# Performance work log

Measured on AMD Instinct MI355X. Metric: run time of the kernel, lower is better.

## Reference

```python
import jax, jax.numpy as jnp
import numpy as np

NUM_HEADS = 16
DIM_HEAD = 64
MAX_LEN = 512


def setup_inputs() -> dict:
    key = jax.random.key(0)
    ks = jax.random.split(key, 6)
    B, N, D = 16, 512, 1024
    inner = NUM_HEADS * DIM_HEAD  # 1024
    x = jax.random.normal(ks[0], (B, N, D), dtype=jnp.float32)
    w_qkv = jax.random.normal(ks[1], (D, 3 * inner), dtype=jnp.float32) * (D ** -0.5)
    b_qkv = jnp.zeros((3 * inner,), dtype=jnp.float32)
    rel_emb = jax.random.normal(ks[2], (2 * MAX_LEN - 1, NUM_HEADS), dtype=jnp.float32) * 0.02
    w_out = jax.random.normal(ks[3], (inner, D), dtype=jnp.float32) * (inner ** -0.5)
    b_out = jnp.zeros((D,), dtype=jnp.float32)
    return {"x": x, "w_qkv": w_qkv, "b_qkv": b_qkv, "rel_emb": rel_emb,
            "w_out": w_out, "b_out": b_out}


def reference(x, w_qkv, b_qkv, rel_emb, w_out, b_out):
    B, N, D = x.shape
    h, dh = NUM_HEADS, DIM_HEAD
    scale = dh ** -0.5
    qkv = x @ w_qkv + b_qkv  # (B, N, 3*h*dh)
    q, k, v = jnp.split(qkv, 3, axis=-1)
    def to_heads(t):
        return t.reshape(B, N, h, dh).transpose(0, 2, 1, 3)  # (B, h, N, dh)
    q, k, v = to_heads(q), to_heads(k), to_heads(v)
    dots = jnp.einsum('bhid,bhjd->bhij', q, k) * scale  # (B, h, N, N)
    # relative position bias: emb[(i - j) + max_len - 1] -> (N, N, h) -> (1, h, N, N)
    idx = jnp.arange(N)[:, None] - jnp.arange(N)[None, :] + (MAX_LEN - 1)
    bias = rel_emb[idx].transpose(2, 0, 1)[None]  # (1, h, N, N)
    attn = jax.nn.softmax(dots + bias, axis=-1)
    out = jnp.einsum('bhij,bhjd->bhid', attn, v)  # (B, h, N, dh)
    out = out.transpose(0, 2, 1, 3).reshape(B, N, h * dh)
    return out @ w_out + b_out
```

## Files before the change

kernel.cpp:

```cpp
#include <hip/hip_runtime.h>

#define SEQ    512
#define NH     16
#define DH     64
#define DMODEL 1024
#define NB     16
#define MROWS  (NB*SEQ)
#define MAXL   512

typedef _Float16 f16;
typedef f16  f16x8 __attribute__((ext_vector_type(8)));
typedef f16  f16x4 __attribute__((ext_vector_type(4)));
typedef float f32x4 __attribute__((ext_vector_type(4)));

__device__ static inline void gll16(const f16* g, f16* l) {
    __builtin_amdgcn_global_load_lds(
        (const __attribute__((address_space(1))) void*)(g),
        (__attribute__((address_space(3))) void*)(l), 16, 0, 0);
}

__global__ __launch_bounds__(256)
void prep(const float* __restrict__ x, f16* __restrict__ xh,
          const float* __restrict__ wqkv, f16* __restrict__ wqkvT,
          const float* __restrict__ wout, f16* __restrict__ woutT)
{
    const int bid = blockIdx.x, t = threadIdx.x;
    if (bid < 8192) {
        int i = (bid * 256 + t) * 4;
        float4 v = *(const float4*)(x + i);
        f16x4 h = { (f16)v.x, (f16)v.y, (f16)v.z, (f16)v.w };
        *(f16x4*)(xh + i) = h;
        return;
    }
    __shared__ float tile[32][33];
    const float* in; f16* out; int C, gx, gy;
    if (bid < 8192 + 3072) {
        int b2 = bid - 8192; in = wqkv; out = wqkvT; C = 3072;
        gx = b2 % 96; gy = b2 / 96;
    } else {
        int b2 = bid - 11264; in = wout; out = woutT; C = 1024;
        gx = b2 & 31; gy = b2 >> 5;
    }
    const int R = 1024;
    int tx = t & 31, ty = t >> 5;
    int c0 = gx * 32, r0 = gy * 32;
    #pragma unroll
    for (int i = 0; i < 4; ++i)
        tile[ty + i * 8][tx] = in[(size_t)(r0 + ty + i * 8) * C + c0 + tx];
    __syncthreads();
    #pragma unroll
    for (int i = 0; i < 4; ++i)
        out[(size_t)(c0 + ty + i * 8) * R + r0 + tx] = (f16)tile[tx][ty + i * 8];
}

template<int MODE>
__global__ __launch_bounds__(256)
void gemm_mfma(const f16* __restrict__ A, const f16* __restrict__ Bt,
               const float* __restrict__ bias, int N, int K,
               float* __restrict__ Cout,
               f16* __restrict__ qb, f16* __restrict__ kb, f16* __restrict__ vb)
{
    __shared__ f16 As[128 * 64];
    __shared__ f16 Bs[128 * 64];
    const int t = threadIdx.x;
    const int lane = t & 63, w = t >> 6;
    const int quad = lane >> 4, l16 = lane & 15;
    const int xr = l16 & 7;
    const int m0 = blockIdx.y * 128, n0 = blockIdx.x * 128;
    const int wm = (w & 1) * 64, wn = (w >> 1) * 64;

    f32x4 acc[4][4];
    #pragma unroll
    for (int i = 0; i < 4; ++i)
        #pragma unroll
        for (int j = 0; j < 4; ++j)
            acc[i][j] = f32x4{0.f, 0.f, 0.f, 0.f};

    const int sr8 = lane >> 3;
    const int sc8 = (lane & 7) ^ sr8;
    const f16* agp = A  + (size_t)(m0 + w * 32 + sr8) * K + sc8 * 8;
    const f16* bgp = Bt + (size_t)(n0 + w * 32 + sr8) * K + sc8 * 8;
    f16* asl = As + w * 2048;
    f16* bsl = Bs + w * 2048;

    for (int k0 = 0; k0 < K; k0 += 64) {
        __syncthreads();
        #pragma unroll
        for (int c = 0; c < 4; ++c) {
            gll16(agp + k0 + c * 8 * K, asl + c * 512);
            gll16(bgp + k0 + c * 8 * K, bsl + c * 512);
        }
        __syncthreads();
        #pragma unroll
        for (int ks = 0; ks < 2; ++ks) {
            f16x8 af[4], bf[4];
            #pragma unroll
            for (int ms = 0; ms < 4; ++ms)
                af[ms] = *(const f16x8*)&As[(wm + ms * 16 + l16) * 64
                                            + (((ks * 4 + quad) ^ xr) * 8)];
            #pragma unroll
            for (int ns = 0; ns < 4; ++ns)
                bf[ns] = *(const f16x8*)&Bs[(wn + ns * 16 + l16) * 64
                                            + (((ks * 4 + quad) ^ xr) * 8)];
            #pragma unroll
            for (int ms = 0; ms < 4; ++ms)
                #pragma unroll
                for (int ns = 0; ns < 4; ++ns)
                    acc[ms][ns] = __builtin_amdgcn_mfma_f32_16x16x32_f16(
                        af[ms], bf[ns], acc[ms][ns], 0, 0, 0);
        }
    }

    if (MODE == 0) {
        #pragma unroll
        for (int ns = 0; ns < 4; ++ns) {
            int col = n0 + wn + ns * 16 + l16;
            float bv = bias[col];
            int which = col >> 10;
            int hh = (col & 1023) >> 6, d = col & 63;
            #pragma unroll
            for (int ms = 0; ms < 4; ++ms) {
                int rowb = m0 + wm + ms * 16 + quad * 4;
                int bb_ = rowb >> 9, n_ = rowb & 511;
                if (which == 0) {
                    #pragma unroll
                    for (int reg = 0; reg < 4; ++reg)
                        qb[((size_t)(bb_ * NH + hh) * SEQ + n_ + reg) * DH + d] =
                            (f16)(acc[ms][ns][reg] + bv);
                } else if (which == 2) {
                    f16x4 pk;
                    #pragma unroll
                    for (int reg = 0; reg < 4; ++reg)
                        pk[reg] = (f16)(acc[ms][ns][reg] + bv);
                    int c8s = ((n_ >> 3) & 7) ^ (d & 7);
                    *(f16x4*)(vb + ((size_t)(bb_ * NH + hh) * DH + d) * SEQ
                                 + (n_ & ~63) + c8s * 8 + (n_ & 7)) = pk;
                } else {
                    #pragma unroll
                    for (int reg = 0; reg < 4; ++reg) {
                        int n = n_ + reg;
                        int dd = (((d >> 3) ^ (n & 7)) * 8) + (d & 7);
                        kb[((size_t)(bb_ * NH + hh) * SEQ + n) * DH + dd] =
                            (f16)(acc[ms][ns][reg] + bv);
                    }
                }
            }
        }
    } else {
        #pragma unroll
        for (int ns = 0; ns < 4; ++ns) {
            int col = n0 + wn + ns * 16 + l16;
            float bv = bias[col];
            #pragma unroll
            for (int ms = 0; ms < 4; ++ms) {
                int rowb = m0 + wm + ms * 16 + quad * 4;
                #pragma unroll
                for (int reg = 0; reg < 4; ++reg)
                    Cout[(size_t)(rowb + reg) * N + col] = acc[ms][ns][reg] + bv;
            }
        }
    }
}

__global__ __launch_bounds__(512)
void attn_mfma(const f16* __restrict__ qb, const f16* __restrict__ kb,
               const f16* __restrict__ vb, const float* __restrict__ rel,
               f16* __restrict__ ob)
{
    __shared__ f16 Ks[128 * 64];
    __shared__ f16 Vt[64 * 128];
    __shared__ f16 Pw[8][16 * 64];
    __shared__ float relh[1024];

    const int t = threadIdx.x;
    const int lane = t & 63, w = t >> 6;
    const int quad = lane >> 4, l16 = lane & 15;
    const int xr = l16 & 7;
    const int bh = blockIdx.x;
    const int h = bh & 15, b = bh >> 4;

    for (int i = t; i < 2 * MAXL - 1; i += 512)
        relh[i] = rel[i * NH + h] * 1.44269504f;

    f16x8 qf[4][2];
    #pragma unroll
    for (int c = 0; c < 4; ++c) {
        const f16* qrow = qb + ((size_t)bh * SEQ + w * 64 + c * 16 + l16) * DH + quad * 8;
        qf[c][0] = *(const f16x8*)(qrow);
        qf[c][1] = *(const f16x8*)(qrow + 32);
    }

    f32x4 o[4][4];
    float lsum[4];
    #pragma unroll
    for (int c = 0; c < 4; ++c) {
        lsum[c] = 0.f;
        #pragma unroll
        for (int dt = 0; dt < 4; ++dt) o[c][dt] = f32x4{0.f, 0.f, 0.f, 0.f};
    }

    const f16* kbase = kb + (size_t)bh * SEQ * DH;
    const f16* vbase = vb + (size_t)bh * DH * SEQ;
    f16* pw = &Pw[w][0];

    for (int kt = 0; kt < 4; ++kt) {
        __syncthreads();
        #pragma unroll
        for (int r = 0; r < 2; ++r) {
            const f16* src = kbase + (size_t)(kt * 128 + r * 64 + w * 8 + (lane >> 3)) * DH
                           + (lane & 7) * 8;
            gll16(src, Ks + r * 4096 + w * 512);
        }
        #pragma unroll
        for (int r = 0; r < 2; ++r) {
            const f16* src = vbase + (size_t)(r * 32 + w * 4 + (lane >> 4)) * SEQ
                           + kt * 128 + ((lane & 15) >> 3) * 64 + (lane & 7) * 8;
            gll16(src, Vt + r * 4096 + w * 512);
        }
        __syncthreads();

        #pragma unroll
        for (int c = 0; c < 4; ++c) {
            f32x4 sT[8];
            #pragma unroll
            for (int mt = 0; mt < 8; ++mt) {
                const f16* kr = &Ks[(mt * 16 + l16) * 64];
                f16x8 a0 = *(const f16x8*)(kr + ((quad ^ xr) * 8));
                f16x8 a1 = *(const f16x8*)(kr + (((4 + quad) ^ xr) * 8));
                f32x4 s = f32x4{0.f, 0.f, 0.f, 0.f};
                s = __builtin_amdgcn_mfma_f32_16x16x32_f16(a0, qf[c][0], s, 0, 0, 0);
                s = __builtin_amdgcn_mfma_f32_16x16x32_f16(a1, qf[c][1], s, 0, 0, 0);
                sT[mt] = s;
            }

            const int cb0 = w * 64 + c * 16 + l16 + (MAXL - 1) - kt * 128 - quad * 4;
            #pragma unroll
            for (int g = 0; g < 2; ++g) {
                #pragma unroll
                for (int m4 = 0; m4 < 4; ++m4) {
                    int mt = g * 4 + m4;
                    f16x4 pk;
                    #pragma unroll
                    for (int reg = 0; reg < 4; ++reg) {
                        float e = exp2f(fmaf(sT[mt][reg], 0.180336878f,
                                             relh[cb0 - mt * 16 - reg]));
                        lsum[c] += e;
                        pk[reg] = (f16)e;
                    }
                    int c8 = (m4 * 2 + (quad >> 1)) ^ xr;
                    *(f16x4*)&pw[l16 * 64 + c8 * 8 + (quad & 1) * 4] = pk;
                }
                __builtin_amdgcn_s_waitcnt(0xC07F);

                #pragma unroll
                for (int s2 = 0; s2 < 2; ++s2) {
                    f16x8 pa = *(const f16x8*)&pw[l16 * 64 + (((s2 * 4 + quad) ^ xr) * 8)];
                    #pragma unroll
                    for (int dt = 0; dt < 4; ++dt) {
                        const f16* vr = &Vt[(dt * 16 + l16) * 128 + g * 64];
                        f16x8 vb8 = *(const f16x8*)(vr + (((s2 * 4 + quad) ^ xr) * 8));
                        o[c][dt] = __builtin_amdgcn_mfma_f32_16x16x32_f16(
                            pa, vb8, o[c][dt], 0, 0, 0);
                    }
                }
            }
        }
    }

    #pragma unroll
    for (int c = 0; c < 4; ++c) {
        float ls = lsum[c];
        ls += __shfl_xor(ls, 16, 64);
        ls += __shfl_xor(ls, 32, 64);
        #pragma unroll
        for (int reg = 0; reg < 4; ++reg) {
            float inv = 1.0f / __shfl(ls, quad * 4 + reg, 64);
            size_t rbase = ((size_t)b * SEQ + w * 64 + c * 16 + quad * 4 + reg) * DMODEL
                         + h * DH;
            #pragma unroll
            for (int dt = 0; dt < 4; ++dt)
                ob[rbase + dt * 16 + l16] = (f16)(o[c][dt][reg] * inv);
        }
    }
}

extern "C" void kernel_launch(void* const* d_in, const int* in_sizes, int n_in,
                              void* d_out, int out_size, void* d_ws, size_t ws_size,
                              hipStream_t stream)
{
    const float* x    = (const float*)d_in[0];
    const float* wqkv = (const float*)d_in[1];
    const float* bqkv = (const float*)d_in[2];
    const float* rel  = (const float*)d_in[3];
    const float* wout = (const float*)d_in[4];
    const float* bout = (const float*)d_in[5];
    float* out = (float*)d_out;
    char* ws = (char*)d_ws;

    const size_t XH = (size_t)MROWS * DMODEL;
    f16* xh    = (f16*)(ws);
    f16* wqkvT = (f16*)(ws + 2 * XH);
    f16* woutT = wqkvT + (size_t)3 * DMODEL * DMODEL;
    f16* qbuf  = woutT + (size_t)DMODEL * DMODEL;
    f16* kbuf  = qbuf + XH;
    f16* vbuf  = kbuf + XH;
    f16* abuf  = vbuf + XH;

    prep<<<12288, 256, 0, stream>>>(x, xh, wqkv, wqkvT, wout, woutT);

    gemm_mfma<0><<<dim3(3 * DMODEL / 128, MROWS / 128), 256, 0, stream>>>(
        xh, wqkvT, bqkv, 3 * DMODEL, DMODEL, nullptr, qbuf, kbuf, vbuf);

    attn_mfma<<<NB * NH, 512, 0, stream>>>(qbuf, kbuf, vbuf, rel, abuf);

    gemm_mfma<1><<<dim3(DMODEL / 128, MROWS / 128), 256, 0, stream>>>(
        abuf, woutT, bout, DMODEL, DMODEL, out, nullptr, nullptr, nullptr);
}
```

Before: 230.1 us.

## Fuse x fp16 conversion into QKV GEMM, use 32x32 MFMA, double-buffer attention K/V

```diff
diff --git a/kernel.cpp b/kernel.cpp
--- a/kernel.cpp
+++ b/kernel.cpp
@@ -11,7 +11,8 @@
 typedef _Float16 f16;
 typedef f16  f16x8 __attribute__((ext_vector_type(8)));
 typedef f16  f16x4 __attribute__((ext_vector_type(4)));
-typedef float f32x4 __attribute__((ext_vector_type(4)));
+typedef float f32x4  __attribute__((ext_vector_type(4)));
+typedef float f32x16 __attribute__((ext_vector_type(16)));
 
 __device__ static inline void gll16(const f16* g, f16* l) {
     __builtin_amdgcn_global_load_lds(
@@ -20,25 +21,17 @@
 }
 
 __global__ __launch_bounds__(256)
-void prep(const float* __restrict__ x, f16* __restrict__ xh,
-          const float* __restrict__ wqkv, f16* __restrict__ wqkvT,
+void prep(const float* __restrict__ wqkv, f16* __restrict__ wqkvT,
           const float* __restrict__ wout, f16* __restrict__ woutT)
 {
     const int bid = blockIdx.x, t = threadIdx.x;
-    if (bid < 8192) {
-        int i = (bid * 256 + t) * 4;
-        float4 v = *(const float4*)(x + i);
-        f16x4 h = { (f16)v.x, (f16)v.y, (f16)v.z, (f16)v.w };
-        *(f16x4*)(xh + i) = h;
-        return;
-    }
     __shared__ float tile[32][33];
     const float* in; f16* out; int C, gx, gy;
-    if (bid < 8192 + 3072) {
-        int b2 = bid - 8192; in = wqkv; out = wqkvT; C = 3072;
-        gx = b2 % 96; gy = b2 / 96;
+    if (bid < 3072) {
+        in = wqkv; out = wqkvT; C = 3072;
+        gx = bid % 96; gy = bid / 96;
     } else {
-        int b2 = bid - 11264; in = wout; out = woutT; C = 1024;
+        int b2 = bid - 3072; in = wout; out = woutT; C = 1024;
         gx = b2 & 31; gy = b2 >> 5;
     }
     const int R = 1024;
@@ -53,9 +46,10 @@
         out[(size_t)(c0 + ty + i * 8) * R + r0 + tx] = (f16)tile[tx][ty + i * 8];
 }
 
-template<int MODE>
+template<int MODE, int CVTA>
 __global__ __launch_bounds__(256)
-void gemm_mfma(const f16* __restrict__ A, const f16* __restrict__ Bt,
+void gemm_mfma(const float* __restrict__ A32, const f16* __restrict__ A16,
+               const f16* __restrict__ Bt,
                const float* __restrict__ bias, int N, int K,
                float* __restrict__ Cout,
                f16* __restrict__ qb, f16* __restrict__ kb, f16* __restrict__ vb)
@@ -64,99 +58,125 @@
     __shared__ f16 Bs[128 * 64];
     const int t = threadIdx.x;
     const int lane = t & 63, w = t >> 6;
-    const int quad = lane >> 4, l16 = lane & 15;
-    const int xr = l16 & 7;
+    const int l32 = lane & 31, half = lane >> 5;
     const int m0 = blockIdx.y * 128, n0 = blockIdx.x * 128;
     const int wm = (w & 1) * 64, wn = (w >> 1) * 64;
 
-    f32x4 acc[4][4];
-    #pragma unroll
-    for (int i = 0; i < 4; ++i)
-        #pragma unroll
-        for (int j = 0; j < 4; ++j)
-            acc[i][j] = f32x4{0.f, 0.f, 0.f, 0.f};
+    f32x16 acc[2][2];
+    #pragma unroll
+    for (int i = 0; i < 2; ++i)
+        #pragma unroll
+        for (int j = 0; j < 2; ++j)
+            acc[i][j] = (f32x16)(0.f);
 
     const int sr8 = lane >> 3;
     const int sc8 = (lane & 7) ^ sr8;
-    const f16* agp = A  + (size_t)(m0 + w * 32 + sr8) * K + sc8 * 8;
     const f16* bgp = Bt + (size_t)(n0 + w * 32 + sr8) * K + sc8 * 8;
+    f16* bsl = Bs + w * 2048;
+    const f16* agp = CVTA ? nullptr
+                          : A16 + (size_t)(m0 + w * 32 + sr8) * K + sc8 * 8;
     f16* asl = As + w * 2048;
-    f16* bsl = Bs + w * 2048;
+
+    const int crow = t >> 1, chalf = t & 1;
+    const float* agp32 = CVTA ? A32 + (size_t)(m0 + crow) * K + chalf * 32 : nullptr;
+    const int cr8 = crow & 7;
 
     for (int k0 = 0; k0 < K; k0 += 64) {
         __syncthreads();
         #pragma unroll
-        for (int c = 0; c < 4; ++c) {
-            gll16(agp + k0 + c * 8 * K, asl + c * 512);
+        for (int c = 0; c < 4; ++c)
             gll16(bgp + k0 + c * 8 * K, bsl + c * 512);
+        if (CVTA) {
+            float4 v[8];
+            #pragma unroll
+            for (int i = 0; i < 8; ++i)
+                v[i] = *(const float4*)(agp32 + k0 + i * 4);
+            #pragma unroll
+            for (int c = 0; c < 4; ++c) {
+                f16x8 hh = { (f16)v[2*c].x, (f16)v[2*c].y, (f16)v[2*c].z, (f16)v[2*c].w,
+                             (f16)v[2*c+1].x, (f16)v[2*c+1].y, (f16)v[2*c+1].z, (f16)v[2*c+1].w };
+                int c8 = (chalf * 4 + c) ^ cr8;
+                *(f16x8*)&As[crow * 64 + c8 * 8] = hh;
+            }
+        } else {
+            #pragma unroll
+            for (int c = 0; c < 4; ++c)
+                gll16(agp + k0 + c * 8 * K, asl + c * 512);
         }
         __syncthreads();
-        #pragma unroll
-        for (int ks = 0; ks < 2; ++ks) {
-            f16x8 af[4], bf[4];
-            #pragma unroll
-            for (int ms = 0; ms < 4; ++ms)
-                af[ms] = *(const f16x8*)&As[(wm + ms * 16 + l16) * 64
-                                            + (((ks * 4 + quad) ^ xr) * 8)];
-            #pragma unroll
-            for (int ns = 0; ns < 4; ++ns)
-                bf[ns] = *(const f16x8*)&Bs[(wn + ns * 16 + l16) * 64
-                                            + (((ks * 4 + quad) ^ xr) * 8)];
-            #pragma unroll
-            for (int ms = 0; ms < 4; ++ms)
-                #pragma unroll
-                for (int ns = 0; ns < 4; ++ns)
-                    acc[ms][ns] = __builtin_amdgcn_mfma_f32_16x16x32_f16(
+
+        #pragma unroll
+        for (int ks = 0; ks < 4; ++ks) {
+            f16x8 af[2], bf[2];
+            #pragma unroll
+            for (int ms = 0; ms < 2; ++ms) {
+                int row = wm + ms * 32 + l32;
+                int c8 = (ks * 2 + half) ^ (row & 7);
+                af[ms] = *(const f16x8*)&As[row * 64 + c8 * 8];
+            }
+            #pragma unroll
+            for (int ns = 0; ns < 2; ++ns) {
+                int row = wn + ns * 32 + l32;
+                int c8 = (ks * 2 + half) ^ (row & 7);
+                bf[ns] = *(const f16x8*)&Bs[row * 64 + c8 * 8];
+            }
+            #pragma unroll
+            for (int ms = 0; ms < 2; ++ms)
+                #pragma unroll
+                for (int ns = 0; ns < 2; ++ns)
+                    acc[ms][ns] = __builtin_amdgcn_mfma_f32_32x32x16_f16(
                         af[ms], bf[ns], acc[ms][ns], 0, 0, 0);
         }
     }
 
-    if (MODE == 0) {
-        #pragma unroll
-        for (int ns = 0; ns < 4; ++ns) {
-            int col = n0 + wn + ns * 16 + l16;
-            float bv = bias[col];
+    const int bb_ = m0 >> 9;
+    #pragma unroll
+    for (int ns = 0; ns < 2; ++ns) {
+        int col = n0 + wn + ns * 32 + l32;
+        float bv = bias[col];
+        if (MODE == 0) {
             int which = col >> 10;
             int hh = (col & 1023) >> 6, d = col & 63;
             #pragma unroll
-            for (int ms = 0; ms < 4; ++ms) {
-                int rowb = m0 + wm + ms * 16 + quad * 4;
-                int bb_ = rowb >> 9, n_ = rowb & 511;
-                if (which == 0) {
-                    #pragma unroll
-                    for (int reg = 0; reg < 4; ++reg)
-                        qb[((size_t)(bb_ * NH + hh) * SEQ + n_ + reg) * DH + d] =
-                            (f16)(acc[ms][ns][reg] + bv);
-                } else if (which == 2) {
-                    f16x4 pk;
-                    #pragma unroll
-                    for (int reg = 0; reg < 4; ++reg)
-                        pk[reg] = (f16)(acc[ms][ns][reg] + bv);
-                    int c8s = ((n_ >> 3) & 7) ^ (d & 7);
-                    *(f16x4*)(vb + ((size_t)(bb_ * NH + hh) * DH + d) * SEQ
-                                 + (n_ & ~63) + c8s * 8 + (n_ & 7)) = pk;
-                } else {
-                    #pragma unroll
-                    for (int reg = 0; reg < 4; ++reg) {
-                        int n = n_ + reg;
-                        int dd = (((d >> 3) ^ (n & 7)) * 8) + (d & 7);
-                        kb[((size_t)(bb_ * NH + hh) * SEQ + n) * DH + dd] =
-                            (f16)(acc[ms][ns][reg] + bv);
+            for (int ms = 0; ms < 2; ++ms) {
+                int rowbase = wm + ms * 32 + 4 * half + (m0 & 511);
+                #pragma unroll
+                for (int g = 0; g < 4; ++g) {
+                    int n_ = rowbase + 8 * g;
+                    if (which == 0) {
+                        #pragma unroll
+                        for (int j = 0; j < 4; ++j)
+                            qb[((size_t)(bb_ * NH + hh) * SEQ + n_ + j) * DH + d] =
+                                (f16)(acc[ms][ns][g * 4 + j] + bv);
+                    } else if (which == 2) {
+                        f16x4 pk;
+                        #pragma unroll
+                        for (int j = 0; j < 4; ++j)
+                            pk[j] = (f16)(acc[ms][ns][g * 4 + j] + bv);
+                        int c8s = ((n_ >> 3) & 7) ^ (d & 7);
+                        *(f16x4*)(vb + ((size_t)(bb_ * NH + hh) * DH + d) * SEQ
+                                     + (n_ & ~63) + c8s * 8 + (n_ & 7)) = pk;
+                    } else {
+                        #pragma unroll
+                        for (int j = 0; j < 4; ++j) {
+                            int n = n_ + j;
+                            int dd = (((d >> 3) ^ (n & 7)) * 8) + (d & 7);
+                            kb[((size_t)(bb_ * NH + hh) * SEQ + n) * DH + dd] =
+                                (f16)(acc[ms][ns][g * 4 + j] + bv);
+                        }
                     }
                 }
             }
-        }
-    } else {
-        #pragma unroll
-        for (int ns = 0; ns < 4; ++ns) {
-            int col = n0 + wn + ns * 16 + l16;
-            float bv = bias[col];
-            #pragma unroll
-            for (int ms = 0; ms < 4; ++ms) {
-                int rowb = m0 + wm + ms * 16 + quad * 4;
-                #pragma unroll
-                for (int reg = 0; reg < 4; ++reg)
-                    Cout[(size_t)(rowb + reg) * N + col] = acc[ms][ns][reg] + bv;
+        } else {
+            #pragma unroll
+            for (int ms = 0; ms < 2; ++ms) {
+                int rowbase = m0 + wm + ms * 32 + 4 * half;
+                #pragma unroll
+                for (int g = 0; g < 4; ++g)
+                    #pragma unroll
+                    for (int j = 0; j < 4; ++j)
+                        Cout[(size_t)(rowbase + 8 * g + j) * N + col] =
+                            acc[ms][ns][g * 4 + j] + bv;
             }
         }
     }
@@ -167,8 +187,8 @@
                const f16* __restrict__ vb, const float* __restrict__ rel,
                f16* __restrict__ ob)
 {
-    __shared__ f16 Ks[128 * 64];
-    __shared__ f16 Vt[64 * 128];
+    __shared__ f16 Ks[2][128 * 64];
+    __shared__ f16 Vt[2][64 * 128];
     __shared__ f16 Pw[8][16 * 64];
     __shared__ float relh[1024];
 
@@ -203,28 +223,35 @@
     const f16* vbase = vb + (size_t)bh * DH * SEQ;
     f16* pw = &Pw[w][0];
 
-    for (int kt = 0; kt < 4; ++kt) {
-        __syncthreads();
+    auto stage = [&](int kt, int buf) {
         #pragma unroll
         for (int r = 0; r < 2; ++r) {
             const f16* src = kbase + (size_t)(kt * 128 + r * 64 + w * 8 + (lane >> 3)) * DH
                            + (lane & 7) * 8;
-            gll16(src, Ks + r * 4096 + w * 512);
+            gll16(src, Ks[buf] + r * 4096 + w * 512);
         }
         #pragma unroll
         for (int r = 0; r < 2; ++r) {
             const f16* src = vbase + (size_t)(r * 32 + w * 4 + (lane >> 4)) * SEQ
                            + kt * 128 + ((lane & 15) >> 3) * 64 + (lane & 7) * 8;
-            gll16(src, Vt + r * 4096 + w * 512);
-        }
-        __syncthreads();
+            gll16(src, Vt[buf] + r * 4096 + w * 512);
+        }
+    };
+
+    stage(0, 0);
+    __syncthreads();
+
+    for (int kt = 0; kt < 4; ++kt) {
+        if (kt < 3) stage(kt + 1, (kt + 1) & 1);
+        const f16* ks = Ks[kt & 1];
+        const f16* vt = Vt[kt & 1];
 
         #pragma unroll
         for (int c = 0; c < 4; ++c) {
             f32x4 sT[8];
             #pragma unroll
             for (int mt = 0; mt < 8; ++mt) {
-                const f16* kr = &Ks[(mt * 16 + l16) * 64];
+                const f16* kr = &ks[(mt * 16 + l16) * 64];
                 f16x8 a0 = *(const f16x8*)(kr + ((quad ^ xr) * 8));
                 f16x8 a1 = *(const f16x8*)(kr + (((4 + quad) ^ xr) * 8));
                 f32x4 s = f32x4{0.f, 0.f, 0.f, 0.f};
@@ -257,7 +284,7 @@
                     f16x8 pa = *(const f16x8*)&pw[l16 * 64 + (((s2 * 4 + quad) ^ xr) * 8)];
                     #pragma unroll
                     for (int dt = 0; dt < 4; ++dt) {
-                        const f16* vr = &Vt[(dt * 16 + l16) * 128 + g * 64];
+                        const f16* vr = &vt[(dt * 16 + l16) * 128 + g * 64];
                         f16x8 vb8 = *(const f16x8*)(vr + (((s2 * 4 + quad) ^ xr) * 8));
                         o[c][dt] = __builtin_amdgcn_mfma_f32_16x16x32_f16(
                             pa, vb8, o[c][dt], 0, 0, 0);
@@ -265,6 +292,7 @@
                 }
             }
         }
+        __syncthreads();
     }
 
     #pragma unroll
@@ -298,21 +326,20 @@
     char* ws = (char*)d_ws;
 
     const size_t XH = (size_t)MROWS * DMODEL;
-    f16* xh    = (f16*)(ws);
-    f16* wqkvT = (f16*)(ws + 2 * XH);
+    f16* wqkvT = (f16*)(ws);
     f16* woutT = wqkvT + (size_t)3 * DMODEL * DMODEL;
     f16* qbuf  = woutT + (size_t)DMODEL * DMODEL;
     f16* kbuf  = qbuf + XH;
     f16* vbuf  = kbuf + XH;
     f16* abuf  = vbuf + XH;
 
-    prep<<<12288, 256, 0, stream>>>(x, xh, wqkv, wqkvT, wout, woutT);
-
-    gemm_mfma<0><<<dim3(3 * DMODEL / 128, MROWS / 128), 256, 0, stream>>>(
-        xh, wqkvT, bqkv, 3 * DMODEL, DMODEL, nullptr, qbuf, kbuf, vbuf);
+    prep<<<4096, 256, 0, stream>>>(wqkv, wqkvT, wout, woutT);
+
+    gemm_mfma<0, 1><<<dim3(3 * DMODEL / 128, MROWS / 128), 256, 0, stream>>>(
+        x, nullptr, wqkvT, bqkv, 3 * DMODEL, DMODEL, nullptr, qbuf, kbuf, vbuf);
 
     attn_mfma<<<NB * NH, 512, 0, stream>>>(qbuf, kbuf, vbuf, rel, abuf);
 
-    gemm_mfma<1><<<dim3(DMODEL / 128, MROWS / 128), 256, 0, stream>>>(
-        abuf, woutT, bout, DMODEL, DMODEL, out, nullptr, nullptr, nullptr);
-}
+    gemm_mfma<1, 0><<<dim3(DMODEL / 128, MROWS / 128), 256, 0, stream>>>(
+        nullptr, abuf, woutT, bout, DMODEL, DMODEL, out, nullptr, nullptr, nullptr);
+}
```

After: 294.9 us. 1.28x slower.
